# Performance work log

Hardware: AMD Instinct MI355X
Metric: run time of the kernel (lower is better)

Reference implementation:

```python
import jax, jax.numpy as jnp
import numpy as np

B, S, D, H = 4, 1024, 1024, 16
QL, KVL = 512, 256
NOPE, ROPE, VD = 64, 32, 64
E, TOPK, FE = 8, 2, 1024  # FE = intermediate_size // expert_num
EPS = 1e-6
NEG = -1e15

def rms_norm(x, w):
    var = jnp.mean(x * x, axis=-1, keepdims=True)
    return w * (x * jax.lax.rsqrt(var + EPS))

def rotate_half(x):
    x1, x2 = jnp.split(x, 2, axis=-1)
    return jnp.concatenate([-x2, x1], axis=-1)

def rope_tables(seq_len, dim):
    inv = 1.0 / (10000.0 ** (np.arange(0, dim, 2, dtype=np.float32) / dim))
    freqs = np.arange(seq_len, dtype=np.float32)[:, None] @ inv[None, :]
    freqs = np.concatenate([freqs, freqs], axis=-1)
    return jnp.asarray(np.cos(freqs)), jnp.asarray(np.sin(freqs))

def setup_inputs():
    key = jax.random.key(0)
    ks = jax.random.split(key, 12)
    s = 0.02
    return {
        'hidden_state': jax.random.normal(ks[0], (B, S, D), jnp.float32),
        'attention_mask': jnp.ones((B, S), jnp.int32),
        'in_ln_w': jnp.ones((D,), jnp.float32),
        'post_ln_w': jnp.ones((D,), jnp.float32),
        'wq_a_w': jax.random.normal(ks[1], (QL, D)) * s,
        'wq_a_b': jnp.zeros((QL,), jnp.float32),
        'q_norm_w': jnp.ones((QL,), jnp.float32),
        'wq_b_w': jax.random.normal(ks[2], (H * (NOPE + ROPE), QL)) * s,
        'wq_b_b': jnp.zeros((H * (NOPE + ROPE),), jnp.float32),
        'wkv_a_w': jax.random.normal(ks[3], (KVL + ROPE, D)) * s,
        'wkv_a_b': jnp.zeros((KVL + ROPE,), jnp.float32),
        'kv_norm_w': jnp.ones((KVL,), jnp.float32),
        'wkv_b_w': jax.random.normal(ks[4], (H * (NOPE + VD), KVL)) * s,
        'wo_w': jax.random.normal(ks[5], (D, H * VD)) * s,
        'wo_b': jnp.zeros((D,), jnp.float32),
        'gate_w': jax.random.normal(ks[6], (E, D)) * s,
        'gate_b': jnp.zeros((E,), jnp.float32),
        'gate_proj': jax.random.normal(ks[7], (E, FE, D)) * s,
        'up_proj': jax.random.normal(ks[8], (E, FE, D)) * s,
        'down_proj': jax.random.normal(ks[9], (E, D, FE)) * s,
    }

def _forward(hidden_state, in_ln_w, post_ln_w, wq_a_w, wq_a_b, q_norm_w, wq_b_w, wq_b_b,
             wkv_a_w, wkv_a_b, kv_norm_w, wkv_b_w, wo_w, wo_b,
             gate_w, gate_b, gate_proj, up_proj, down_proj, attention_mask):
    x = rms_norm(hidden_state, in_ln_w)
    # ---- MLA ----
    q = rms_norm(x @ wq_a_w.T + wq_a_b, q_norm_w)
    q = (q @ wq_b_w.T + wq_b_b).reshape(B, S, H, NOPE + ROPE)
    q_nope, q_pe = q[..., :NOPE], q[..., NOPE:]
    kvp = x @ wkv_a_w.T + wkv_a_b
    kv, k_pe = kvp[..., :KVL], kvp[..., KVL:]
    kv = rms_norm(kv, kv_norm_w)
    cos, sin = rope_tables(S, ROPE)
    cos = cos[None, :, None, :]
    sin = sin[None, :, None, :]
    q_pe = q_pe * cos + rotate_half(q_pe) * sin            # [B,S,H,ROPE]
    k_pe = k_pe[:, :, None, :]
    k_pe = (k_pe * cos + rotate_half(k_pe) * sin)[:, :, 0]  # [B,S,ROPE]
    # kv_cache / pe_cache are filled with detached copies in the original
    kv_c = jax.lax.stop_gradient(kv)
    pe_c = jax.lax.stop_gradient(k_pe)
    wkv_b = wkv_b_w.reshape(H, NOPE + VD, KVL)
    q_abs = jnp.einsum('bshd,hdc->bshc', q_nope, wkv_b[:, :NOPE])  # cache-absorption
    scores = (jnp.einsum('bshc,btc->bsht', q_abs, kv_c)
              + jnp.einsum('bshr,btr->bsht', q_pe, pe_c)) / np.float32(np.sqrt(NOPE + ROPE))
    causal = jnp.triu(jnp.full((S, S), NEG, dtype=scores.dtype), 1)
    mask = jnp.where((attention_mask == 0)[:, None, :], NEG, causal[None])  # [B,S,S]
    scores = scores + mask[:, :, None, :]
    probs = jax.nn.softmax(scores, axis=-1)
    o = jnp.einsum('bsht,btc->bshc', probs, kv_c)
    o = jnp.einsum('bshc,hdc->bshd', o, wkv_b[:, NOPE:])
    attn = o.reshape(B, S, H * VD) @ wo_w.T + wo_b
    h = attn + hidden_state
    # ---- MoE ----
    y = rms_norm(h, post_ln_w)
    logits = y @ gate_w.T + gate_b                                   # [B,S,E]
    _, idx = jax.lax.top_k(logits, TOPK)
    sel = jnp.any(jax.nn.one_hot(idx, E, dtype=bool), axis=-2)       # [B,S,E]
    sparse = jax.nn.softmax(jnp.where(sel, logits, -jnp.inf), axis=-1)  # zeros off top-k
    g = jax.nn.silu(jnp.einsum('bsd,efd->bsef', y, gate_proj))
    u = jnp.einsum('bsd,efd->bsef', y, up_proj)
    eo = jnp.einsum('bsef,edf->bsed', g * u, down_proj)
    moe_out = jnp.einsum('bsed,bse->bsd', eo, sparse)
    out = moe_out + h
    return out, logits.reshape(-1, E)

def reference(hidden_state, attention_mask, in_ln_w, post_ln_w, wq_a_w, wq_a_b, q_norm_w,
              wq_b_w, wq_b_b, wkv_a_w, wkv_a_b, kv_norm_w, wkv_b_w, wo_w, wo_b,
              gate_w, gate_b, gate_proj, up_proj, down_proj):
    return _forward(hidden_state, in_ln_w, post_ln_w, wq_a_w, wq_a_b, q_norm_w, wq_b_w, wq_b_b,
                    wkv_a_w, wkv_a_b, kv_norm_w, wkv_b_w, wo_w, wo_b,
                    gate_w, gate_b, gate_proj, up_proj, down_proj, attention_mask)
```

## Files before the change

kernel.cpp:

```cpp
#include <hip/hip_runtime.h>
#include <math.h>

#define NB   4
#define NS   1024
#define ND   1024
#define NH   16
#define NTOK 4096
#define NFE  1024
#define ETOK_CAP 10240

#define SCL_LOG2E 0.14724445f

static constexpr size_t OFF_GWP  = 0;
static constexpr size_t OFF_TKW  = 8192;
static constexpr size_t OFF_EW   = 16384;
static constexpr size_t OFF_INT  = 26624;
static constexpr size_t OFF_X    = 45184;
static constexpr size_t OFF_QA   = 2142336;
static constexpr size_t OFF_GATE = 2142336;
static constexpr size_t OFF_UP   = 6336640;
static constexpr size_t OFF_QAB  = 8433792;
static constexpr size_t OFF_KVP  = 9482368;
static constexpr size_t OFF_KVC  = 10662016;
static constexpr size_t OFF_WA   = 11251840;
// ... 106 lines not shown
#pragma unroll
    for (int j = 0; j < 4; j++) acc[i][j] = (f32x4_t){0.f, 0.f, 0.f, 0.f};

  ld(0); st();
  __syncthreads();
  for (int k0 = 0; ; ) {
    int kn = k0 + 64;
    if (kn < K) ld(kn);
#pragma unroll
    for (int kk = 0; kk < 2; kk++) {
      bf16x8_t af[4], wf[4];
#pragma unroll
      for (int i = 0; i < 4; i++)
        af[i] = *(const bf16x8_t*)&As[(mw + 16*i + lr) * GSTR + kk*32 + lg*8];
#pragma unroll
      for (int j = 0; j < 4; j++)
        wf[j] = *(const bf16x8_t*)&Ws2[(nw + 16*j + lr) * GSTR + kk*32 + lg*8];
#pragma unroll
      for (int i = 0; i < 4; i++)
#pragma unroll
        for (int j = 0; j < 4; j++)
          acc[i][j] = __builtin_amdgcn_mfma_f32_16x16x32_bf16(af[i], wf[j], acc[i][j], 0, 0, 0);
    }
    k0 = kn;
    if (k0 >= K) break;
    __syncthreads();
    st();
    __syncthreads();
  }
#pragma unroll
  for (int j = 0; j < 4; j++) {
    int n = n0 + nw + 16*j + lr;
    if (n < N) {
      float bv = bias[n];
#pragma unroll
      for (int i = 0; i < 4; i++) {
#pragma unroll
        for (int r = 0; r < 4; r++) {
          int m = m0 + mw + 16*i + 4*lg + r;
          size_t off = (size_t)m * ldc + n;
          float v = acc[i][j][r] + bv;
          if (RESID) v += resid[off];
          if (OUTBF) ((unsigned short*)Cv)[off] = f2bfs(v);
          else       ((float*)Cv)[off] = v;
        }
      }
    }
  }
}

__global__ __launch_bounds__(256) void rope_q_kernel(float* qbuf)
{
  int id = blockIdx.x * 256 + threadIdx.x;
  int d = id & 15;
  int h = (id >> 4) & 15;
  int sr = id >> 8;
  int s = sr & (NS - 1);
  float inv = __expf(-(float)(2 * d) * (9.210340371976184f / 32.f));
  float fr = (float)s * inv;
  float sn, cs; sincosf(fr, &sn, &cs);
  float* p = qbuf + (size_t)sr * 1536 + h * 96 + 64;
  float x1 = p[d], x2 = p[d + 16];
  p[d]      = x1 * cs - x2 * sn;
  p[d + 16] = x2 * cs + x1 * sn;
}

__global__ __launch_bounds__(256) void rope_k_kernel(const float* kvp, unsigned short* kvc)
{
  int id = blockIdx.x * 256 + threadIdx.x;
  int d = id & 15;
  int sr = id >> 4;
  int s = sr & (NS - 1);
  float inv = __expf(-(float)(2 * d) * (9.210340371976184f / 32.f));
  float fr = (float)s * inv;
  float sn, cs; sincosf(fr, &sn, &cs);
  const float* src = kvp + (size_t)sr * 288 + 256;
  unsigned short* dst = kvc + (size_t)sr * 288 + 256;
  float x1 = src[d], x2 = src[d + 16];
  dst[d]      = f2bfs(x1 * cs - x2 * sn);
  dst[d + 16] = f2bfs(x2 * cs + x1 * sn);
}

#define KSTR 296
#define QNSTR 65
#define VPAD 40
#define OSTR2 132

__global__ __launch_bounds__(256, 2) void attn_kernel(
    const float* __restrict__ qbuf,
    const unsigned short* __restrict__ kvc,
    const float* __restrict__ wkvb,
    unsigned short* __restrict__ oproj)
{
  extern __shared__ float4 smem_f4[];
  unsigned short* sm  = (unsigned short*)smem_f4;
  unsigned short* ks  = sm;
  unsigned short* vt  = sm + 9472;
  unsigned short* ps  = sm + 19712;
  float* qn           = (float*)sm;
  unsigned short* qst = sm + 8320;
  float* o_lds        = (float*)sm;

  int bx = blockIdx.x;
  int h = blockIdx.y, b = blockIdx.z;
  int t = threadIdx.x;
  int lane = t & 63, wv_ = t >> 6;
  int lrow = lane & 15, lg = lane >> 4;
  int qrow = 16 * wv_ + lrow;

  int srow[5], sc16[5];
#pragma unroll
  for (int it = 0; it < 5; it++) {
    int c = it * 256 + t;
    srow[it] = c / 36; sc16[it] = c % 36;
  }
  bool tail = (t < 128);

  for (int half = 0; half < 2; half++) {
    int qb = half ? bx : (15 - bx);
    int row0 = b * NS + qb * 64;
    __syncthreads();

    for (int idx = t; idx < 4096; idx += 256) {
      int r = idx >> 6, c = idx & 63;
      qn[r * QNSTR + c] = qbuf[(size_t)(row0 + r) * 1536 + h * 96 + c] * SCL_LOG2E;
    }
    bf16x8_t bq[9];
    {
      const float* src = qbuf + (size_t)(row0 + qrow) * 1536 + h * 96 + 64 + lg * 8;
      unsigned short* bp = (unsigned short*)&bq[8];
#pragma unroll
      for (int j = 0; j < 8; j++) bp[j] = f2bfs(src[j] * SCL_LOG2E);
    }
    __syncthreads();
    {
      int cx = t & 63, ry = t >> 6;
      float a[16][4] = {};
      const float* wb = wkvb + (size_t)h * 32768 + cx * 4;
      for (int k = 0; k < 64; k++) {
        float4 wv = *(const float4*)(wb + (size_t)k * 256);
#pragma unroll
        for (int r = 0; r < 16; r++) {
          float qv = qn[(ry * 16 + r) * QNSTR + k];
          a[r][0] += qv * wv.x; a[r][1] += qv * wv.y; a[r][2] += qv * wv.z; a[r][3] += qv * wv.w;
        }
      }
      __syncthreads();
#pragma unroll
      for (int r = 0; r < 16; r++) {
        uint2 pk; pk.x = pack2(a[r][0], a[r][1]); pk.y = pack2(a[r][2], a[r][3]);
        *(uint2*)&qst[(ry * 16 + r) * KSTR + cx * 4] = pk;
      }
    }
    __syncthreads();
#pragma unroll
    for (int kk = 0; kk < 8; kk++)
      bq[kk] = *(const bf16x8_t*)&qst[qrow * KSTR + kk * 32 + lg * 8];
    __syncthreads();

    float m_run = -1e30f, l_run = 0.f;
    f32x4_t acco[16];
#pragma unroll
    for (int n = 0; n < 16; n++) acco[n] = (f32x4_t){0.f, 0.f, 0.f, 0.f};

    uint4 pa[5];
    unsigned short vg[32];

    auto issue = [&](int kb2) {
      const unsigned short* tb = kvc + ((size_t)b * NS + kb2 * 32) * 288;
#pragma unroll
      for (int it = 0; it < 4; it++)
        pa[it] = *(const uint4*)(tb + srow[it] * 288 + sc16[it] * 8);
      if (tail) pa[4] = *(const uint4*)(tb + srow[4] * 288 + sc16[4] * 8);
      const unsigned short* vsrc = tb + t;
#pragma unroll
      for (int k = 0; k < 32; k++) vg[k] = vsrc[k * 288];
    };
    auto commit = [&]() {
#pragma unroll
      for (int it = 0; it < 5; it++) {
        if (it == 4 && !tail) continue;
        *(uint4*)&ks[srow[it] * KSTR + sc16[it] * 8] = pa[it];
      }
      unsigned wds[16];
#pragma unroll
      for (int j = 0; j < 16; j++)
        wds[j] = (unsigned)vg[2*j] | ((unsigned)vg[2*j+1] << 16);
#pragma unroll
      for (int j = 0; j < 4; j++)
        *(uint4*)&vt[t * VPAD + j * 8] =
          make_uint4(wds[4*j], wds[4*j+1], wds[4*j+2], wds[4*j+3]);
    };

    int nkb = 2 * qb + 2;
    issue(0); commit();
    __syncthreads();
    for (int kb = 0; kb < nkb; kb++) {
      bool more = (kb + 1 < nkb);
      if (more) issue(kb + 1);
      int key0 = kb * 32;
      f32x4_t s0e = {0.f,0.f,0.f,0.f}, s0o = {0.f,0.f,0.f,0.f};
      f32x4_t s1e = {0.f,0.f,0.f,0.f}, s1o = {0.f,0.f,0.f,0.f};
#pragma unroll
      for (int kk = 0; kk < 9; kk++) {
        bf16x8_t a0 = *(const bf16x8_t*)&ks[lrow * KSTR + kk*32 + lg*8];
        bf16x8_t a1 = *(const bf16x8_t*)&ks[(16 + lrow) * KSTR + kk*32 + lg*8];
        if (kk & 1) {
          s0o = __builtin_amdgcn_mfma_f32_16x16x32_bf16(a0, bq[kk], s0o, 0, 0, 0);
          s1o = __builtin_amdgcn_mfma_f32_16x16x32_bf16(a1, bq[kk], s1o, 0, 0, 0);
        } else {
          s0e = __builtin_amdgcn_mfma_f32_16x16x32_bf16(a0, bq[kk], s0e, 0, 0, 0);
          s1e = __builtin_amdgcn_mfma_f32_16x16x32_bf16(a1, bq[kk], s1e, 0, 0, 0);
        }
      }
      f32x4_t s0a = s0e + s0o, s1a = s1e + s1o;
      int qg = qb * 64 + qrow;
      float sv[8];
      if (key0 + 31 > qb * 64 + 16 * wv_) {
#pragma unroll
        for (int r = 0; r < 4; r++) {
          sv[r]     = (key0 + 4*lg + r      <= qg) ? s0a[r] : -1e30f;
          sv[4 + r] = (key0 + 16 + 4*lg + r <= qg) ? s1a[r] : -1e30f;
        }
      } else {
#pragma unroll
        for (int r = 0; r < 4; r++) { sv[r] = s0a[r]; sv[4 + r] = s1a[r]; }
      }
      float mx = sv[0];
#pragma unroll
      for (int i = 1; i < 8; i++) mx = fmaxf(mx, sv[i]);
      mx = fmaxf(mx, __shfl_xor(mx, 16));
      mx = fmaxf(mx, __shfl_xor(mx, 32));
      if (!__all(mx - m_run <= 11.0f)) {
        float mnew = fmaxf(m_run, mx);
        float al = exp2f(m_run - mnew);
        m_run = mnew;
        l_run *= al;
        float al0 = __shfl(al, 4*lg + 0);
        float al1 = __shfl(al, 4*lg + 1);
        float al2 = __shfl(al, 4*lg + 2);
        float al3 = __shfl(al, 4*lg + 3);
#pragma unroll
        for (int n = 0; n < 16; n++) {
          acco[n][0] *= al0; acco[n][1] *= al1; acco[n][2] *= al2; acco[n][3] *= al3;
        }
      }
      float sum = 0.f;
#pragma unroll
      for (int i = 0; i < 8; i++) { sv[i] = exp2f(sv[i] - m_run); sum += sv[i]; }
      sum += __shfl_xor(sum, 16);
      sum += __shfl_xor(sum, 32);
      l_run += sum;
      {
        int swz = qrow & 3;
        int g0 = lg >> 1, h0 = lg & 1;
        uint2 p0; p0.x = pack2(sv[0], sv[1]); p0.y = pack2(sv[2], sv[3]);
        uint2 p1; p1.x = pack2(sv[4], sv[5]); p1.y = pack2(sv[6], sv[7]);
        char* pr = (char*)ps + qrow * 64;
        *(uint2*)(pr + ((g0 ^ swz) * 16 + h0 * 8))       = p0;
        *(uint2*)(pr + (((2 + g0) ^ swz) * 16 + h0 * 8)) = p1;
      }
      {
        bf16x8_t ap = *(const bf16x8_t*)((char*)ps + qrow * 64 + ((lg ^ (qrow & 3)) * 16));
#pragma unroll
        for (int n = 0; n < 16; n++) {
          bf16x8_t bv = *(const bf16x8_t*)&vt[(16*n + lrow) * VPAD + lg * 8];
          acco[n] = __builtin_amdgcn_mfma_f32_16x16x32_bf16(ap, bv, acco[n], 0, 0, 0);
        }
      }
      __syncthreads();
      if (more) { commit(); __syncthreads(); }
    }
    float li = 1.f / l_run;
    float l0 = __shfl(li, 4*lg + 0);
    float l1 = __shfl(li, 4*lg + 1);
    float l2 = __shfl(li, 4*lg + 2);
    float l3 = __shfl(li, 4*lg + 3);
    int dx = t & 15, ty2 = t >> 4;
    float pr[4][4] = {};
    const float* wb2 = wkvb + (size_t)(h * 128 + 64) * 256;
#pragma unroll
    for (int p = 0; p < 2; p++) {
      __syncthreads();
#pragma unroll
      for (int n = 8*p; n < 8*p + 8; n++) {
        int fc = 16*n + lrow - 128*p;
        o_lds[(16*wv_ + 4*lg + 0) * OSTR2 + fc] = acco[n][0] * l0;
        o_lds[(16*wv_ + 4*lg + 1) * OSTR2 + fc] = acco[n][1] * l1;
        o_lds[(16*wv_ + 4*lg + 2) * OSTR2 + fc] = acco[n][2] * l2;
        o_lds[(16*wv_ + 4*lg + 3) * OSTR2 + fc] = acco[n][3] * l3;
      }
      __syncthreads();
      for (int c = 0; c < 128; c += 4) {
        float4 w0 = *(const float4*)(wb2 + (size_t)(dx*4 + 0) * 256 + 128*p + c);
        float4 w1 = *(const float4*)(wb2 + (size_t)(dx*4 + 1) * 256 + 128*p + c);
        float4 w2 = *(const float4*)(wb2 + (size_t)(dx*4 + 2) * 256 + 128*p + c);
        float4 w3 = *(const float4*)(wb2 + (size_t)(dx*4 + 3) * 256 + 128*p + c);
#pragma unroll
        for (int i = 0; i < 4; i++) {
          float4 ov = *(const float4*)&o_lds[(ty2*4 + i) * OSTR2 + c];
          pr[i][0] += ov.x*w0.x + ov.y*w0.y + ov.z*w0.z + ov.w*w0.w;
          pr[i][1] += ov.x*w1.x + ov.y*w1.y + ov.z*w1.z + ov.w*w1.w;
          pr[i][2] += ov.x*w2.x + ov.y*w2.y + ov.z*w2.z + ov.w*w2.w;
          pr[i][3] += ov.x*w3.x + ov.y*w3.y + ov.z*w3.z + ov.w*w3.w;
        }
      }
    }
#pragma unroll
    for (int i = 0; i < 4; i++)
#pragma unroll
      for (int j = 0; j < 4; j++)
        oproj[(size_t)(row0 + ty2*4 + i) * 1024 + h * 64 + dx*4 + j] = f2bfs(pr[i][j]);
  }
}

__global__ __launch_bounds__(256) void gate_kernel(
    const float* __restrict__ H, const float* __restrict__ gwp,
    const float* __restrict__ gb, float* __restrict__ logits)
{
  __shared__ __align__(16) float ly[1024];
  __shared__ float red[4];
  int tok = blockIdx.x, t = threadIdx.x;
  float4 hv = *(const float4*)(H + (size_t)tok * ND + t * 4);
  *(float4*)&ly[t * 4] = hv;
  float ss = hv.x*hv.x + hv.y*hv.y + hv.z*hv.z + hv.w*hv.w;
#pragma unroll
  for (int k = 1; k < 64; k <<= 1) ss += __shfl_xor(ss, k);
  if ((t & 63) == 0) red[t >> 6] = ss;
  __syncthreads();
  float inv = rsqrtf((red[0] + red[1] + red[2] + red[3]) * (1.f / 1024.f) + 1e-6f);
  int e = t >> 5, lane = t & 31;
  const float* w = gwp + (size_t)e * ND;
  float acc = 0.f;
  for (int d = lane; d < ND; d += 32) acc += ly[d] * w[d];
#pragma unroll
  for (int k = 16; k >= 1; k >>= 1) acc += __shfl_xor(acc, k);
  if (lane == 0) logits[(size_t)tok * 8 + e] = acc * inv + gb[e];
}

__global__ __launch_bounds__(256) void topk_kernel(
    const float* __restrict__ logits, int* __restrict__ tke,
    float* __restrict__ tkw, int* __restrict__ cnt)
{
  int tok = blockIdx.x * 256 + threadIdx.x;
  if (tok >= NTOK) return;
  float l[8];
#pragma unroll
  for (int e2 = 0; e2 < 8; e2++) l[e2] = logits[(size_t)tok * 8 + e2];
  float v0 = l[0]; int e0 = 0;
#pragma unroll
  for (int e2 = 1; e2 < 8; e2++) if (l[e2] > v0) { v0 = l[e2]; e0 = e2; }
  float v1 = -INFINITY; int e1 = 0;
#pragma unroll
  for (int e2 = 0; e2 < 8; e2++) if (e2 != e0 && l[e2] > v1) { v1 = l[e2]; e1 = e2; }
  float x = __expf(v1 - v0);
  float w0 = 1.f / (1.f + x);
  tke[tok * 2]     = e0; tke[tok * 2 + 1] = e1;
  tkw[tok * 2]     = w0; tkw[tok * 2 + 1] = 1.f - w0;
  atomicAdd(&cnt[e0], 1);
  atomicAdd(&cnt[8 + e1], 1);
}

__global__ void offsets_kernel(const int* cnt, int* base, int* pcnt)
{
  if (threadIdx.x == 0 && blockIdx.x == 0) {
    int cum = 0;
    for (int s2 = 0; s2 < 16; s2++) {
      int p = (cnt[s2] + 127) & ~127;
      base[s2] = cum; pcnt[s2] = p; cum += p;
    }
  }
}

__global__ __launch_bounds__(256) void scatter_kernel(
    const int* __restrict__ tke, const float* __restrict__ tkw,
    const int* __restrict__ base, int* cnt2,
    int* __restrict__ etok, float* __restrict__ ew)
{
  int tok = blockIdx.x * 256 + threadIdx.x;
  if (tok >= NTOK) return;
#pragma unroll
  for (int k = 0; k < 2; k++) {
    int e = tke[tok * 2 + k];
    int seg = k * 8 + e;
    int pos = atomicAdd(&cnt2[seg], 1);
    int row = base[seg] + pos;
    etok[row] = tok;
    ew[row] = tkw[tok * 2 + k];
  }
}

#define MSTR 40

__global__ __launch_bounds__(256) void moe_mlp1_mfma(
    const unsigned short* __restrict__ Y,
    const unsigned short* __restrict__ Gp, const unsigned short* __restrict__ Up,
    const int* __restrict__ etok, const int* __restrict__ base,
    const int* __restrict__ pcnt, unsigned short* __restrict__ act)
{
  int seg = blockIdx.z;
  if ((int)(blockIdx.y * 128) >= pcnt[seg]) return;
  int e = seg & 7;
  __shared__ __align__(16) unsigned short As[128 * MSTR];
  __shared__ __align__(16) unsigned short Gs[128 * MSTR];
  __shared__ __align__(16) unsigned short Us[128 * MSTR];
  int t = threadIdx.x;
  int row0 = base[seg] + blockIdx.y * 128;
  int n0 = blockIdx.x * 128;
  int lane = t & 63, w = t >> 6;
  int mw = (w >> 1) * 64, nw = (w & 1) * 64;
  int lr = lane & 15, lg = lane >> 4;

  int srowv[2], sc8v[2];
#pragma unroll
  for (int it = 0; it < 2; it++) { int c = it*256 + t; srowv[it] = c >> 2; sc8v[it] = (c & 3) * 8; }
  int tokr[2];
#pragma unroll
  for (int it = 0; it < 2; it++) tokr[it] = etok[row0 + srowv[it]];

  uint4 pa[2], pg[2], pu[2];
  auto ld = [&](int k0) {
#pragma unroll
    for (int it = 0; it < 2; it++) {
      pa[it] = (tokr[it] >= 0)
        ? *(const uint4*)(Y + (size_t)tokr[it] * ND + k0 + sc8v[it])
        : make_uint4(0u, 0u, 0u, 0u);
      pg[it] = *(const uint4*)(Gp + ((size_t)e * NFE + n0 + srowv[it]) * ND + k0 + sc8v[it]);
      pu[it] = *(const uint4*)(Up + ((size_t)e * NFE + n0 + srowv[it]) * ND + k0 + sc8v[it]);
    }
  };
  auto st = [&]() {
#pragma unroll
    for (int it = 0; it < 2; it++) {
      *(uint4*)&As[srowv[it] * MSTR + sc8v[it]] = pa[it];
      *(uint4*)&Gs[srowv[it] * MSTR + sc8v[it]] = pg[it];
      *(uint4*)&Us[srowv[it] * MSTR + sc8v[it]] = pu[it];
    }
  };

  f32x4_t accg[4][4], accu[4][4];
#pragma unroll
  for (int i = 0; i < 4; i++)
#pragma unroll
    for (int j = 0; j < 4; j++) {
      accg[i][j] = (f32x4_t){0.f, 0.f, 0.f, 0.f};
      accu[i][j] = (f32x4_t){0.f, 0.f, 0.f, 0.f};
    }

  ld(0); st();
  __syncthreads();
  for (int k0 = 0; ; ) {
    int kn = k0 + 32;
    if (kn < ND) ld(kn);
    bf16x8_t af[4], gf[4], uf[4];
#pragma unroll
    for (int i = 0; i < 4; i++)
      af[i] = *(const bf16x8_t*)&As[(mw + 16*i + lr) * MSTR + lg*8];
#pragma unroll
    for (int j = 0; j < 4; j++) {
      gf[j] = *(const bf16x8_t*)&Gs[(nw + 16*j + lr) * MSTR + lg*8];
      uf[j] = *(const bf16x8_t*)&Us[(nw + 16*j + lr) * MSTR + lg*8];
    }
#pragma unroll
    for (int i = 0; i < 4; i++)
#pragma unroll
      for (int j = 0; j < 4; j++) {
        accg[i][j] = __builtin_amdgcn_mfma_f32_16x16x32_bf16(af[i], gf[j], accg[i][j], 0, 0, 0);
        accu[i][j] = __builtin_amdgcn_mfma_f32_16x16x32_bf16(af[i], uf[j], accu[i][j], 0, 0, 0);
      }
    k0 = kn;
    if (k0 >= ND) break;
    __syncthreads();
    st();
    __syncthreads();
  }
#pragma unroll
  for (int i = 0; i < 4; i++)
#pragma unroll
    for (int j = 0; j < 4; j++) {
      int n = n0 + nw + 16*j + lr;
#pragma unroll
      for (int r = 0; r < 4; r++) {
        int m = row0 + mw + 16*i + 4*lg + r;
        float g = accg[i][j][r], u = accu[i][j][r];
        float s = g / (1.f + __expf(-g));
        act[(size_t)m * NFE + n] = f2bfs(s * u);
      }
    }
}

__global__ __launch_bounds__(256) void moe_down_mfma(
    const unsigned short* __restrict__ act, const unsigned short* __restrict__ Dp,
    const int* __restrict__ etok, const float* __restrict__ ew,
    const int* __restrict__ base, const int* __restrict__ pcnt,
    int slot, float* __restrict__ out)
{
  int e = blockIdx.z;
  int seg = slot * 8 + e;
  if ((int)(blockIdx.y * 128) >= pcnt[seg]) return;
  __shared__ __align__(16) unsigned short As[128 * GSTR];
  __shared__ __align__(16) unsigned short Ws2[128 * GSTR];
  int t = threadIdx.x;
  int row0 = base[seg] + blockIdx.y * 128;
  int n0 = blockIdx.x * 128;
  int lane = t & 63, w = t >> 6;
  int mw = (w >> 1) * 64, nw = (w & 1) * 64;
  int lr = lane & 15, lg = lane >> 4;

  int srowv[4], sc8v[4];
#pragma unroll
  for (int it = 0; it < 4; it++) { int c = it*256 + t; srowv[it] = c >> 3; sc8v[it] = (c & 7) * 8; }

  uint4 pa[4], pw[4];
  auto ld = [&](int k0) {
#pragma unroll
    for (int it = 0; it < 4; it++) {
      pa[it] = *(const uint4*)(act + (size_t)(row0 + srowv[it]) * NFE + k0 + sc8v[it]);
      pw[it] = *(const uint4*)(Dp + ((size_t)e * ND + n0 + srowv[it]) * NFE + k0 + sc8v[it]);
    }
  };
  auto st = [&]() {
#pragma unroll
    for (int it = 0; it < 4; it++) {
      *(uint4*)&As[srowv[it] * GSTR + sc8v[it]] = pa[it];
      *(uint4*)&Ws2[srowv[it] * GSTR + sc8v[it]] = pw[it];
    }
  };

  f32x4_t acc[4][4];
#pragma unroll
  for (int i = 0; i < 4; i++)
#pragma unroll
    for (int j = 0; j < 4; j++) acc[i][j] = (f32x4_t){0.f, 0.f, 0.f, 0.f};

  ld(0); st();
  __syncthreads();
  for (int k0 = 0; ; ) {
    int kn = k0 + 64;
    if (kn < NFE) ld(kn);
#pragma unroll
    for (int kk = 0; kk < 2; kk++) {
      bf16x8_t af[4], wf[4];
#pragma unroll
      for (int i = 0; i < 4; i++)
        af[i] = *(const bf16x8_t*)&As[(mw + 16*i + lr) * GSTR + kk*32 + lg*8];
#pragma unroll
      for (int j = 0; j < 4; j++)
        wf[j] = *(const bf16x8_t*)&Ws2[(nw + 16*j + lr) * GSTR + kk*32 + lg*8];
#pragma unroll
      for (int i = 0; i < 4; i++)
#pragma unroll
        for (int j = 0; j < 4; j++)
          acc[i][j] = __builtin_amdgcn_mfma_f32_16x16x32_bf16(af[i], wf[j], acc[i][j], 0, 0, 0);
    }
    k0 = kn;
    if (k0 >= NFE) break;
    __syncthreads();
    st();
    __syncthreads();
  }
#pragma unroll
  for (int i = 0; i < 4; i++) {
// ... 10 lines not shown
      for (int r = 0; r < 4; r++) {
        if (tks[r] >= 0)
          out[(size_t)tks[r] * ND + n] += ews[r] * acc[i][j][r];
      }
    }
  }
}

extern "C" void kernel_launch(void* const* d_in, const int* in_sizes, int n_in,
                              void* d_out, int out_size, void* d_ws, size_t ws_size,
                              hipStream_t stream) {
  const float* hidden    = (const float*)d_in[0];
  const float* in_ln_w   = (const float*)d_in[2];
  const float* post_ln_w = (const float*)d_in[3];
  const float* wq_a_w    = (const float*)d_in[4];
  const float* wq_a_b    = (const float*)d_in[5];
  const float* q_norm_w  = (const float*)d_in[6];
  const float* wq_b_w    = (const float*)d_in[7];
  const float* wq_b_b    = (const float*)d_in[8];
  const float* wkv_a_w   = (const float*)d_in[9];
  const float* wkv_a_b   = (const float*)d_in[10];
  const float* kv_norm_w = (const float*)d_in[11];
  const float* wkv_b_w   = (const float*)d_in[12];
  const float* wo_w      = (const float*)d_in[13];
  const float* wo_b      = (const float*)d_in[14];
  const float* gate_w    = (const float*)d_in[15];
  const float* gate_b    = (const float*)d_in[16];
  const float* gate_proj = (const float*)d_in[17];
  const float* up_proj   = (const float*)d_in[18];
  const float* down_proj = (const float*)d_in[19];

  float* ws = (float*)d_ws;
  if (ws_size < WS_FLOATS * sizeof(float)) return;

  float* gwp = ws + OFF_GWP;
  float* tkw = ws + OFF_TKW;
  float* ew  = ws + OFF_EW;
  int* ib   = (int*)(ws + OFF_INT);
  int* tke  = ib;
  int* etok = ib + 8192;
  int* cnt  = ib + 8192 + ETOK_CAP;
  int* cnt2 = cnt + 16;
  int* base = cnt + 32;
  int* pcnt = cnt + 48;

  unsigned short* x_bf   = (unsigned short*)(ws + OFF_X);
  unsigned short* oproj  = (unsigned short*)(ws + OFF_X);
  unsigned short* ybuf   = (unsigned short*)(ws + OFF_X);
  float*          qa     = ws + OFF_QA;
  float*          qbuf   = ws + OFF_QA;
  unsigned short* gate_bf= (unsigned short*)(ws + OFF_GATE);
  unsigned short* down_bf= (unsigned short*)(ws + OFF_GATE);
  unsigned short* up_bf  = (unsigned short*)(ws + OFF_UP);
  unsigned short* qab    = (unsigned short*)(ws + OFF_QAB);
  float*          kvp    = ws + OFF_KVP;
  unsigned short* kvc    = (unsigned short*)(ws + OFF_KVC);
  unsigned short* actb   = (unsigned short*)(ws + OFF_ACT);
  unsigned short* wqa_bf = (unsigned short*)(ws + OFF_WA + WA_WQA);
  unsigned short* wqb_bf = (unsigned short*)(ws + OFF_WA + WA_WQB);
  unsigned short* wkva_bf= (unsigned short*)(ws + OFF_WA + WA_WKVA);
  unsigned short* wo_bf  = (unsigned short*)(ws + OFF_WA + WA_WO);

  float* out    = (float*)d_out;
  float* logits = out + (size_t)NTOK * ND;

  conv_bf16_kernel<<<256, 256, 0, stream>>>(wq_a_w, wqa_bf, 524288);
  conv_bf16_kernel<<<144, 256, 0, stream>>>(wkv_a_w, wkva_bf, 294912);
  conv_bf16_kernel<<<384, 256, 0, stream>>>(wq_b_w, wqb_bf, 786432);
  conv_bf16_kernel<<<512, 256, 0, stream>>>(wo_w, wo_bf, 1048576);
  conv_gwp_kernel<<<32, 256, 0, stream>>>(gate_w, post_ln_w, gwp);

  rmsnorm_bf16<4><<<NTOK, 256, 0, stream>>>(hidden, ND, in_ln_w, x_bf, ND);
  gemm_bf16<false,false><<<dim3(4, 32), 256, 0, stream>>>(
      x_bf, ND, wqa_bf, ND, wq_a_b, nullptr, qa, 512, 512, ND);
  gemm_bf16<false,false><<<dim3(3, 32), 256, 0, stream>>>(
      x_bf, ND, wkva_bf, ND, wkv_a_b, nullptr, kvp, 288, 288, ND);
  rmsnorm_bf16<2><<<NTOK, 256, 0, stream>>>(qa, 512, q_norm_w, qab, 512);
  rmsnorm_bf16<1><<<NTOK, 256, 0, stream>>>(kvp, 288, kv_norm_w, kvc, 288);
  gemm_bf16<false,false><<<dim3(12, 32), 256, 0, stream>>>(
      qab, 512, wqb_bf, 512, wq_b_b, nullptr, qbuf, 1536, 1536, 512);
  rope_q_kernel<<<4096, 256, 0, stream>>>(qbuf);
  rope_k_kernel<<<256, 256, 0, stream>>>(kvp, kvc);
  {
    size_t smem = 54528;
    hipFuncSetAttribute((const void*)attn_kernel,
                        hipFuncAttributeMaxDynamicSharedMemorySize, (int)smem);
    attn_kernel<<<dim3(8, NH, NB), 256, smem, stream>>>(qbuf, kvc, wkv_b_w, oproj);
  }
  conv_bf16_kernel<<<4096, 256, 0, stream>>>(gate_proj, gate_bf, 8388608);
  conv_bf16_kernel<<<4096, 256, 0, stream>>>(up_proj, up_bf, 8388608);
  gemm_bf16<false,true><<<dim3(8, 32), 256, 0, stream>>>(
      oproj, ND, wo_bf, ND, wo_b, hidden, out, ND, ND, ND);
  rmsnorm_bf16<4><<<NTOK, 256, 0, stream>>>(out, ND, post_ln_w, ybuf, ND);
  gate_kernel<<<NTOK, 256, 0, stream>>>(out, gwp, gate_b, logits);
  hipMemsetAsync(cnt, 0, 32 * sizeof(int), stream);
  hipMemsetAsync(etok, 0xFF, ETOK_CAP * sizeof(int), stream);
  topk_kernel<<<16, 256, 0, stream>>>(logits, tke, tkw, cnt);
  offsets_kernel<<<1, 64, 0, stream>>>(cnt, base, pcnt);
  scatter_kernel<<<16, 256, 0, stream>>>(tke, tkw, base, cnt2, etok, ew);
  moe_mlp1_mfma<<<dim3(8, 32, 16), 256, 0, stream>>>(ybuf, gate_bf, up_bf,
                                                     etok, base, pcnt, actb);
  conv_bf16_kernel<<<4096, 256, 0, stream>>>(down_proj, down_bf, 8388608);
  moe_down_mfma<<<dim3(8, 32, 8), 256, 0, stream>>>(actb, down_bf, etok, ew,
                                                    base, pcnt, 0, out);
  moe_down_mfma<<<dim3(8, 32, 8), 256, 0, stream>>>(actb, down_bf, etok, ew,
                                                    base, pcnt, 1, out);
}
```

Baseline: 1.012 ms.

## Split attention blocks to one query tile each and retile MoE gate/up GEMM

The attention kernel no longer pairs two causal query tiles per block. It launches one block per 64-row query tile and raises the occupancy hint to 3 blocks per CU, relying on the reversed tile order for load balance. The q-norm staging stride drops its padding, which may add LDS bank conflicts. The MoE gate/up kernel moves from 128x128 to 128x64 N-tiles with a 64-wide K step, so twice as many blocks launch with fewer accumulators each, but the activation tile is reloaded across more N-blocks.

```diff
diff --git a/kernel.cpp b/kernel.cpp
--- a/kernel.cpp
+++ b/kernel.cpp
@@ -212,11 +212,11 @@
 }
 
 #define KSTR 296
-#define QNSTR 65
+#define QNSTR 64
 #define VPAD 40
 #define OSTR2 132
 
-__global__ __launch_bounds__(256, 2) void attn_kernel(
+__global__ __launch_bounds__(256, 3) void attn_kernel(
     const float* __restrict__ qbuf,
     const unsigned short* __restrict__ kvc,
     const float* __restrict__ wkvb,
@@ -228,16 +228,58 @@
   unsigned short* vt  = sm + 9472;
   unsigned short* ps  = sm + 19712;
   float* qn           = (float*)sm;
-  unsigned short* qst = sm + 8320;
+  unsigned short* qst = sm + 8192;
   float* o_lds        = (float*)sm;
 
-  int bx = blockIdx.x;
+  int qb = (NS / 64 - 1) - blockIdx.x;
   int h = blockIdx.y, b = blockIdx.z;
   int t = threadIdx.x;
+  int row0 = b * NS + qb * 64;
   int lane = t & 63, wv_ = t >> 6;
   int lrow = lane & 15, lg = lane >> 4;
   int qrow = 16 * wv_ + lrow;
 
+  for (int idx = t; idx < 4096; idx += 256) {
+    int r = idx >> 6, c = idx & 63;
+    qn[r * QNSTR + c] = qbuf[(size_t)(row0 + r) * 1536 + h * 96 + c] * SCL_LOG2E;
+  }
+  bf16x8_t bq[9];
+  {
+    const float* src = qbuf + (size_t)(row0 + qrow) * 1536 + h * 96 + 64 + lg * 8;
+    unsigned short* bp = (unsigned short*)&bq[8];
+#pragma unroll
+    for (int j = 0; j < 8; j++) bp[j] = f2bfs(src[j] * SCL_LOG2E);
+  }
+  __syncthreads();
+  {
+    int cx = t & 63, ry = t >> 6;
+    float a[16][4] = {};
+    const float* wb = wkvb + (size_t)h * 32768 + cx * 4;
+    for (int k = 0; k < 64; k++) {
+      float4 wv = *(const float4*)(wb + (size_t)k * 256);
+#pragma unroll
+      for (int r = 0; r < 16; r++) {
+        float qv = qn[(ry * 16 + r) * QNSTR + k];
+        a[r][0] += qv * wv.x; a[r][1] += qv * wv.y; a[r][2] += qv * wv.z; a[r][3] += qv * wv.w;
+      }
+    }
+#pragma unroll
+    for (int r = 0; r < 16; r++) {
+      uint2 pk; pk.x = pack2(a[r][0], a[r][1]); pk.y = pack2(a[r][2], a[r][3]);
+      *(uint2*)&qst[(ry * 16 + r) * KSTR + cx * 4] = pk;
+    }
+  }
+  __syncthreads();
+#pragma unroll
+  for (int kk = 0; kk < 8; kk++)
+    bq[kk] = *(const bf16x8_t*)&qst[qrow * KSTR + kk * 32 + lg * 8];
+  __syncthreads();
+
+  float m_run = -1e30f, l_run = 0.f;
+  f32x4_t acco[16];
+#pragma unroll
+  for (int n = 0; n < 16; n++) acco[n] = (f32x4_t){0.f, 0.f, 0.f, 0.f};
+
   int srow[5], sc16[5];
 #pragma unroll
   for (int it = 0; it < 5; it++) {
@@ -245,203 +287,154 @@
     srow[it] = c / 36; sc16[it] = c % 36;
   }
   bool tail = (t < 128);
-
-  for (int half = 0; half < 2; half++) {
-    int qb = half ? bx : (15 - bx);
-    int row0 = b * NS + qb * 64;
+  uint4 pa[5];
+  unsigned short vg[32];
+
+  auto issue = [&](int kb2) {
+    const unsigned short* tb = kvc + ((size_t)b * NS + kb2 * 32) * 288;
+#pragma unroll
+    for (int it = 0; it < 4; it++)
+      pa[it] = *(const uint4*)(tb + srow[it] * 288 + sc16[it] * 8);
+    if (tail) pa[4] = *(const uint4*)(tb + srow[4] * 288 + sc16[4] * 8);
+    const unsigned short* vsrc = tb + t;
+#pragma unroll
+    for (int k = 0; k < 32; k++) vg[k] = vsrc[k * 288];
+  };
+  auto commit = [&]() {
+#pragma unroll
+    for (int it = 0; it < 5; it++) {
+      if (it == 4 && !tail) continue;
+      *(uint4*)&ks[srow[it] * KSTR + sc16[it] * 8] = pa[it];
+    }
+    unsigned wds[16];
+#pragma unroll
+    for (int j = 0; j < 16; j++)
+      wds[j] = (unsigned)vg[2*j] | ((unsigned)vg[2*j+1] << 16);
+#pragma unroll
+    for (int j = 0; j < 4; j++)
+      *(uint4*)&vt[t * VPAD + j * 8] =
+        make_uint4(wds[4*j], wds[4*j+1], wds[4*j+2], wds[4*j+3]);
+  };
+
+  int nkb = 2 * qb + 2;
+  issue(0); commit();
+  __syncthreads();
+  for (int kb = 0; kb < nkb; kb++) {
+    bool more = (kb + 1 < nkb);
+    if (more) issue(kb + 1);
+    int key0 = kb * 32;
+    f32x4_t s0e = {0.f,0.f,0.f,0.f}, s0o = {0.f,0.f,0.f,0.f};
+    f32x4_t s1e = {0.f,0.f,0.f,0.f}, s1o = {0.f,0.f,0.f,0.f};
+#pragma unroll
+    for (int kk = 0; kk < 9; kk++) {
+      bf16x8_t a0 = *(const bf16x8_t*)&ks[lrow * KSTR + kk*32 + lg*8];
+      bf16x8_t a1 = *(const bf16x8_t*)&ks[(16 + lrow) * KSTR + kk*32 + lg*8];
+      if (kk & 1) {
+        s0o = __builtin_amdgcn_mfma_f32_16x16x32_bf16(a0, bq[kk], s0o, 0, 0, 0);
+        s1o = __builtin_amdgcn_mfma_f32_16x16x32_bf16(a1, bq[kk], s1o, 0, 0, 0);
+      } else {
+        s0e = __builtin_amdgcn_mfma_f32_16x16x32_bf16(a0, bq[kk], s0e, 0, 0, 0);
+        s1e = __builtin_amdgcn_mfma_f32_16x16x32_bf16(a1, bq[kk], s1e, 0, 0, 0);
+      }
+    }
+    f32x4_t s0a = s0e + s0o, s1a = s1e + s1o;
+    int qg = qb * 64 + qrow;
+    float sv[8];
+    if (key0 + 31 > qb * 64 + 16 * wv_) {
+#pragma unroll
+      for (int r = 0; r < 4; r++) {
+        sv[r]     = (key0 + 4*lg + r      <= qg) ? s0a[r] : -1e30f;
+        sv[4 + r] = (key0 + 16 + 4*lg + r <= qg) ? s1a[r] : -1e30f;
+      }
+    } else {
+#pragma unroll
+      for (int r = 0; r < 4; r++) { sv[r] = s0a[r]; sv[4 + r] = s1a[r]; }
+    }
+    float mx = sv[0];
+#pragma unroll
+    for (int i = 1; i < 8; i++) mx = fmaxf(mx, sv[i]);
+    mx = fmaxf(mx, __shfl_xor(mx, 16));
+    mx = fmaxf(mx, __shfl_xor(mx, 32));
+    if (!__all(mx - m_run <= 11.0f)) {
+      float mnew = fmaxf(m_run, mx);
+      float al = exp2f(m_run - mnew);
+      m_run = mnew;
+      l_run *= al;
+      float al0 = __shfl(al, 4*lg + 0);
+      float al1 = __shfl(al, 4*lg + 1);
+      float al2 = __shfl(al, 4*lg + 2);
+      float al3 = __shfl(al, 4*lg + 3);
+#pragma unroll
+      for (int n = 0; n < 16; n++) {
+        acco[n][0] *= al0; acco[n][1] *= al1; acco[n][2] *= al2; acco[n][3] *= al3;
+      }
+    }
+    float sum = 0.f;
+#pragma unroll
+    for (int i = 0; i < 8; i++) { sv[i] = exp2f(sv[i] - m_run); sum += sv[i]; }
+    sum += __shfl_xor(sum, 16);
+    sum += __shfl_xor(sum, 32);
+    l_run += sum;
+    {
+      int swz = qrow & 3;
+      int g0 = lg >> 1, h0 = lg & 1;
+      uint2 p0; p0.x = pack2(sv[0], sv[1]); p0.y = pack2(sv[2], sv[3]);
+      uint2 p1; p1.x = pack2(sv[4], sv[5]); p1.y = pack2(sv[6], sv[7]);
+      char* pr = (char*)ps + qrow * 64;
+      *(uint2*)(pr + ((g0 ^ swz) * 16 + h0 * 8))       = p0;
+      *(uint2*)(pr + (((2 + g0) ^ swz) * 16 + h0 * 8)) = p1;
+    }
+    {
+      bf16x8_t ap = *(const bf16x8_t*)((char*)ps + qrow * 64 + ((lg ^ (qrow & 3)) * 16));
+#pragma unroll
+      for (int n = 0; n < 16; n++) {
+        bf16x8_t bv = *(const bf16x8_t*)&vt[(16*n + lrow) * VPAD + lg * 8];
+        acco[n] = __builtin_amdgcn_mfma_f32_16x16x32_bf16(ap, bv, acco[n], 0, 0, 0);
+      }
+    }
     __syncthreads();
-
-    for (int idx = t; idx < 4096; idx += 256) {
-      int r = idx >> 6, c = idx & 63;
-      qn[r * QNSTR + c] = qbuf[(size_t)(row0 + r) * 1536 + h * 96 + c] * SCL_LOG2E;
-    }
-    bf16x8_t bq[9];
-    {
-      const float* src = qbuf + (size_t)(row0 + qrow) * 1536 + h * 96 + 64 + lg * 8;
-      unsigned short* bp = (unsigned short*)&bq[8];
-#pragma unroll
-      for (int j = 0; j < 8; j++) bp[j] = f2bfs(src[j] * SCL_LOG2E);
-    }
+    if (more) { commit(); __syncthreads(); }
+  }
+  float li = 1.f / l_run;
+  float l0 = __shfl(li, 4*lg + 0);
+  float l1 = __shfl(li, 4*lg + 1);
+  float l2 = __shfl(li, 4*lg + 2);
+  float l3 = __shfl(li, 4*lg + 3);
+  int dx = t & 15, ty2 = t >> 4;
+  float pr[4][4] = {};
+  const float* wb2 = wkvb + (size_t)(h * 128 + 64) * 256;
+#pragma unroll
+  for (int p = 0; p < 2; p++) {
     __syncthreads();
-    {
-      int cx = t & 63, ry = t >> 6;
-      float a[16][4] = {};
-      const float* wb = wkvb + (size_t)h * 32768 + cx * 4;
-      for (int k = 0; k < 64; k++) {
-        float4 wv = *(const float4*)(wb + (size_t)k * 256);
-#pragma unroll
-        for (int r = 0; r < 16; r++) {
-          float qv = qn[(ry * 16 + r) * QNSTR + k];
-          a[r][0] += qv * wv.x; a[r][1] += qv * wv.y; a[r][2] += qv * wv.z; a[r][3] += qv * wv.w;
-        }
-      }
-      __syncthreads();
-#pragma unroll
-      for (int r = 0; r < 16; r++) {
-        uint2 pk; pk.x = pack2(a[r][0], a[r][1]); pk.y = pack2(a[r][2], a[r][3]);
-        *(uint2*)&qst[(ry * 16 + r) * KSTR + cx * 4] = pk;
-      }
+#pragma unroll
+    for (int n = 8*p; n < 8*p + 8; n++) {
+      int fc = 16*n + lrow - 128*p;
+      o_lds[(16*wv_ + 4*lg + 0) * OSTR2 + fc] = acco[n][0] * l0;
+      o_lds[(16*wv_ + 4*lg + 1) * OSTR2 + fc] = acco[n][1] * l1;
+      o_lds[(16*wv_ + 4*lg + 2) * OSTR2 + fc] = acco[n][2] * l2;
+      o_lds[(16*wv_ + 4*lg + 3) * OSTR2 + fc] = acco[n][3] * l3;
     }
     __syncthreads();
-#pragma unroll
-    for (int kk = 0; kk < 8; kk++)
-      bq[kk] = *(const bf16x8_t*)&qst[qrow * KSTR + kk * 32 + lg * 8];
-    __syncthreads();
-
-    float m_run = -1e30f, l_run = 0.f;
-    f32x4_t acco[16];
-#pragma unroll
-    for (int n = 0; n < 16; n++) acco[n] = (f32x4_t){0.f, 0.f, 0.f, 0.f};
-
-    uint4 pa[5];
-    unsigned short vg[32];
-
-    auto issue = [&](int kb2) {
-      const unsigned short* tb = kvc + ((size_t)b * NS + kb2 * 32) * 288;
-#pragma unroll
-      for (int it = 0; it < 4; it++)
-        pa[it] = *(const uint4*)(tb + srow[it] * 288 + sc16[it] * 8);
-      if (tail) pa[4] = *(const uint4*)(tb + srow[4] * 288 + sc16[4] * 8);
-      const unsigned short* vsrc = tb + t;
-#pragma unroll
-      for (int k = 0; k < 32; k++) vg[k] = vsrc[k * 288];
-    };
-    auto commit = [&]() {
-#pragma unroll
-      for (int it = 0; it < 5; it++) {
-        if (it == 4 && !tail) continue;
-        *(uint4*)&ks[srow[it] * KSTR + sc16[it] * 8] = pa[it];
-      }
-      unsigned wds[16];
-#pragma unroll
-      for (int j = 0; j < 16; j++)
-        wds[j] = (unsigned)vg[2*j] | ((unsigned)vg[2*j+1] << 16);
-#pragma unroll
-      for (int j = 0; j < 4; j++)
-        *(uint4*)&vt[t * VPAD + j * 8] =
-          make_uint4(wds[4*j], wds[4*j+1], wds[4*j+2], wds[4*j+3]);
-    };
-
-    int nkb = 2 * qb + 2;
-    issue(0); commit();
-    __syncthreads();
-    for (int kb = 0; kb < nkb; kb++) {
-      bool more = (kb + 1 < nkb);
-      if (more) issue(kb + 1);
-      int key0 = kb * 32;
-      f32x4_t s0e = {0.f,0.f,0.f,0.f}, s0o = {0.f,0.f,0.f,0.f};
-      f32x4_t s1e = {0.f,0.f,0.f,0.f}, s1o = {0.f,0.f,0.f,0.f};
-#pragma unroll
-      for (int kk = 0; kk < 9; kk++) {
-        bf16x8_t a0 = *(const bf16x8_t*)&ks[lrow * KSTR + kk*32 + lg*8];
-        bf16x8_t a1 = *(const bf16x8_t*)&ks[(16 + lrow) * KSTR + kk*32 + lg*8];
-        if (kk & 1) {
-          s0o = __builtin_amdgcn_mfma_f32_16x16x32_bf16(a0, bq[kk], s0o, 0, 0, 0);
-          s1o = __builtin_amdgcn_mfma_f32_16x16x32_bf16(a1, bq[kk], s1o, 0, 0, 0);
-        } else {
-          s0e = __builtin_amdgcn_mfma_f32_16x16x32_bf16(a0, bq[kk], s0e, 0, 0, 0);
-          s1e = __builtin_amdgcn_mfma_f32_16x16x32_bf16(a1, bq[kk], s1e, 0, 0, 0);
-        }
-      }
-      f32x4_t s0a = s0e + s0o, s1a = s1e + s1o;
-      int qg = qb * 64 + qrow;
-      float sv[8];
-      if (key0 + 31 > qb * 64 + 16 * wv_) {
-#pragma unroll
-        for (int r = 0; r < 4; r++) {
-          sv[r]     = (key0 + 4*lg + r      <= qg) ? s0a[r] : -1e30f;
-          sv[4 + r] = (key0 + 16 + 4*lg + r <= qg) ? s1a[r] : -1e30f;
-        }
-      } else {
-#pragma unroll
-        for (int r = 0; r < 4; r++) { sv[r] = s0a[r]; sv[4 + r] = s1a[r]; }
-      }
-      float mx = sv[0];
-#pragma unroll
-      for (int i = 1; i < 8; i++) mx = fmaxf(mx, sv[i]);
-      mx = fmaxf(mx, __shfl_xor(mx, 16));
-      mx = fmaxf(mx, __shfl_xor(mx, 32));
-      if (!__all(mx - m_run <= 11.0f)) {
-        float mnew = fmaxf(m_run, mx);
-        float al = exp2f(m_run - mnew);
-        m_run = mnew;
-        l_run *= al;
-        float al0 = __shfl(al, 4*lg + 0);
-        float al1 = __shfl(al, 4*lg + 1);
-        float al2 = __shfl(al, 4*lg + 2);
-        float al3 = __shfl(al, 4*lg + 3);
-#pragma unroll
-        for (int n = 0; n < 16; n++) {
-          acco[n][0] *= al0; acco[n][1] *= al1; acco[n][2] *= al2; acco[n][3] *= al3;
-        }
-      }
-      float sum = 0.f;
-#pragma unroll
-      for (int i = 0; i < 8; i++) { sv[i] = exp2f(sv[i] - m_run); sum += sv[i]; }
-      sum += __shfl_xor(sum, 16);
-      sum += __shfl_xor(sum, 32);
-      l_run += sum;
-      {
-        int swz = qrow & 3;
-        int g0 = lg >> 1, h0 = lg & 1;
-        uint2 p0; p0.x = pack2(sv[0], sv[1]); p0.y = pack2(sv[2], sv[3]);
-        uint2 p1; p1.x = pack2(sv[4], sv[5]); p1.y = pack2(sv[6], sv[7]);
-        char* pr = (char*)ps + qrow * 64;
-        *(uint2*)(pr + ((g0 ^ swz) * 16 + h0 * 8))       = p0;
-        *(uint2*)(pr + (((2 + g0) ^ swz) * 16 + h0 * 8)) = p1;
-      }
-      {
-        bf16x8_t ap = *(const bf16x8_t*)((char*)ps + qrow * 64 + ((lg ^ (qrow & 3)) * 16));
-#pragma unroll
-        for (int n = 0; n < 16; n++) {
-          bf16x8_t bv = *(const bf16x8_t*)&vt[(16*n + lrow) * VPAD + lg * 8];
-          acco[n] = __builtin_amdgcn_mfma_f32_16x16x32_bf16(ap, bv, acco[n], 0, 0, 0);
-        }
-      }
-      __syncthreads();
-      if (more) { commit(); __syncthreads(); }
-    }
-    float li = 1.f / l_run;
-    float l0 = __shfl(li, 4*lg + 0);
-    float l1 = __shfl(li, 4*lg + 1);
-    float l2 = __shfl(li, 4*lg + 2);
-    float l3 = __shfl(li, 4*lg + 3);
-    int dx = t & 15, ty2 = t >> 4;
-    float pr[4][4] = {};
-    const float* wb2 = wkvb + (size_t)(h * 128 + 64) * 256;
-#pragma unroll
-    for (int p = 0; p < 2; p++) {
-      __syncthreads();
-#pragma unroll
-      for (int n = 8*p; n < 8*p + 8; n++) {
-        int fc = 16*n + lrow - 128*p;
-        o_lds[(16*wv_ + 4*lg + 0) * OSTR2 + fc] = acco[n][0] * l0;
-        o_lds[(16*wv_ + 4*lg + 1) * OSTR2 + fc] = acco[n][1] * l1;
-        o_lds[(16*wv_ + 4*lg + 2) * OSTR2 + fc] = acco[n][2] * l2;
-        o_lds[(16*wv_ + 4*lg + 3) * OSTR2 + fc] = acco[n][3] * l3;
-      }
-      __syncthreads();
-      for (int c = 0; c < 128; c += 4) {
-        float4 w0 = *(const float4*)(wb2 + (size_t)(dx*4 + 0) * 256 + 128*p + c);
-        float4 w1 = *(const float4*)(wb2 + (size_t)(dx*4 + 1) * 256 + 128*p + c);
-        float4 w2 = *(const float4*)(wb2 + (size_t)(dx*4 + 2) * 256 + 128*p + c);
-        float4 w3 = *(const float4*)(wb2 + (size_t)(dx*4 + 3) * 256 + 128*p + c);
-#pragma unroll
-        for (int i = 0; i < 4; i++) {
-          float4 ov = *(const float4*)&o_lds[(ty2*4 + i) * OSTR2 + c];
-          pr[i][0] += ov.x*w0.x + ov.y*w0.y + ov.z*w0.z + ov.w*w0.w;
-          pr[i][1] += ov.x*w1.x + ov.y*w1.y + ov.z*w1.z + ov.w*w1.w;
-          pr[i][2] += ov.x*w2.x + ov.y*w2.y + ov.z*w2.z + ov.w*w2.w;
-          pr[i][3] += ov.x*w3.x + ov.y*w3.y + ov.z*w3.z + ov.w*w3.w;
-        }
-      }
-    }
-#pragma unroll
-    for (int i = 0; i < 4; i++)
-#pragma unroll
-      for (int j = 0; j < 4; j++)
-        oproj[(size_t)(row0 + ty2*4 + i) * 1024 + h * 64 + dx*4 + j] = f2bfs(pr[i][j]);
-  }
+    for (int c = 0; c < 128; c += 4) {
+      float4 w0 = *(const float4*)(wb2 + (size_t)(dx*4 + 0) * 256 + 128*p + c);
+      float4 w1 = *(const float4*)(wb2 + (size_t)(dx*4 + 1) * 256 + 128*p + c);
+      float4 w2 = *(const float4*)(wb2 + (size_t)(dx*4 + 2) * 256 + 128*p + c);
+      float4 w3 = *(const float4*)(wb2 + (size_t)(dx*4 + 3) * 256 + 128*p + c);
+#pragma unroll
+      for (int i = 0; i < 4; i++) {
+        float4 ov = *(const float4*)&o_lds[(ty2*4 + i) * OSTR2 + c];
+        pr[i][0] += ov.x*w0.x + ov.y*w0.y + ov.z*w0.z + ov.w*w0.w;
+        pr[i][1] += ov.x*w1.x + ov.y*w1.y + ov.z*w1.z + ov.w*w1.w;
+        pr[i][2] += ov.x*w2.x + ov.y*w2.y + ov.z*w2.z + ov.w*w2.w;
+        pr[i][3] += ov.x*w3.x + ov.y*w3.y + ov.z*w3.z + ov.w*w3.w;
+      }
+    }
+  }
+#pragma unroll
+  for (int i = 0; i < 4; i++)
+#pragma unroll
+    for (int j = 0; j < 4; j++)
+      oproj[(size_t)(row0 + ty2*4 + i) * 1024 + h * 64 + dx*4 + j] = f2bfs(pr[i][j]);
 }
 
 __global__ __launch_bounds__(256) void gate_kernel(
@@ -520,9 +513,7 @@
   }
 }
 
-#define MSTR 40
-
-__global__ __launch_bounds__(256) void moe_mlp1_mfma(
+__global__ __launch_bounds__(256, 3) void moe_mlp1_mfma(
     const unsigned short* __restrict__ Y,
     const unsigned short* __restrict__ Gp, const unsigned short* __restrict__ Up,
     const int* __restrict__ etok, const int* __restrict__ base,
@@ -531,48 +522,51 @@
   int seg = blockIdx.z;
   if ((int)(blockIdx.y * 128) >= pcnt[seg]) return;
   int e = seg & 7;
-  __shared__ __align__(16) unsigned short As[128 * MSTR];
-  __shared__ __align__(16) unsigned short Gs[128 * MSTR];
-  __shared__ __align__(16) unsigned short Us[128 * MSTR];
+  __shared__ __align__(16) unsigned short As[128 * GSTR];
+  __shared__ __align__(16) unsigned short Gs[64 * GSTR];
+  __shared__ __align__(16) unsigned short Us[64 * GSTR];
   int t = threadIdx.x;
   int row0 = base[seg] + blockIdx.y * 128;
-  int n0 = blockIdx.x * 128;
+  int n0 = blockIdx.x * 64;
   int lane = t & 63, w = t >> 6;
-  int mw = (w >> 1) * 64, nw = (w & 1) * 64;
+  int mw = (w >> 1) * 64, nw = (w & 1) * 32;
   int lr = lane & 15, lg = lane >> 4;
 
-  int srowv[2], sc8v[2];
-#pragma unroll
-  for (int it = 0; it < 2; it++) { int c = it*256 + t; srowv[it] = c >> 2; sc8v[it] = (c & 3) * 8; }
-  int tokr[2];
-#pragma unroll
-  for (int it = 0; it < 2; it++) tokr[it] = etok[row0 + srowv[it]];
-
-  uint4 pa[2], pg[2], pu[2];
+  int srow = t >> 3, sc8 = (t & 7) * 8;
+  int tokr[4];
+#pragma unroll
+  for (int it = 0; it < 4; it++) tokr[it] = etok[row0 + it*32 + srow];
+
+  uint4 pa[4], pg[2], pu[2];
   auto ld = [&](int k0) {
 #pragma unroll
+    for (int it = 0; it < 4; it++)
+      pa[it] = (tokr[it] >= 0)
+        ? *(const uint4*)(Y + (size_t)tokr[it] * ND + k0 + sc8)
+        : make_uint4(0u, 0u, 0u, 0u);
+#pragma unroll
     for (int it = 0; it < 2; it++) {
-      pa[it] = (tokr[it] >= 0)
-        ? *(const uint4*)(Y + (size_t)tokr[it] * ND + k0 + sc8v[it])
-        : make_uint4(0u, 0u, 0u, 0u);
-      pg[it] = *(const uint4*)(Gp + ((size_t)e * NFE + n0 + srowv[it]) * ND + k0 + sc8v[it]);
-      pu[it] = *(const uint4*)(Up + ((size_t)e * NFE + n0 + srowv[it]) * ND + k0 + sc8v[it]);
+      int r = n0 + it*32 + srow;
+      pg[it] = *(const uint4*)(Gp + ((size_t)e * NFE + r) * ND + k0 + sc8);
+      pu[it] = *(const uint4*)(Up + ((size_t)e * NFE + r) * ND + k0 + sc8);
     }
   };
   auto st = [&]() {
 #pragma unroll
+    for (int it = 0; it < 4; it++)
+      *(uint4*)&As[(it*32 + srow) * GSTR + sc8] = pa[it];
+#pragma unroll
     for (int it = 0; it < 2; it++) {
-      *(uint4*)&As[srowv[it] * MSTR + sc8v[it]] = pa[it];
-      *(uint4*)&Gs[srowv[it] * MSTR + sc8v[it]] = pg[it];
-      *(uint4*)&Us[srowv[it] * MSTR + sc8v[it]] = pu[it];
+      *(uint4*)&Gs[(it*32 + srow) * GSTR + sc8] = pg[it];
+      *(uint4*)&Us[(it*32 + srow) * GSTR + sc8] = pu[it];
     }
   };
 
-  f32x4_t accg[4][4], accu[4][4];
+  f32x4_t accg[4][2], accu[4][2];
 #pragma unroll
   for (int i = 0; i < 4; i++)
 #pragma unroll
-    for (int j = 0; j < 4; j++) {
+    for (int j = 0; j < 2; j++) {
       accg[i][j] = (f32x4_t){0.f, 0.f, 0.f, 0.f};
       accu[i][j] = (f32x4_t){0.f, 0.f, 0.f, 0.f};
     }
@@ -580,24 +574,27 @@
   ld(0); st();
   __syncthreads();
   for (int k0 = 0; ; ) {
-    int kn = k0 + 32;
+    int kn = k0 + 64;
     if (kn < ND) ld(kn);
-    bf16x8_t af[4], gf[4], uf[4];
-#pragma unroll
-    for (int i = 0; i < 4; i++)
-      af[i] = *(const bf16x8_t*)&As[(mw + 16*i + lr) * MSTR + lg*8];
-#pragma unroll
-    for (int j = 0; j < 4; j++) {
-      gf[j] = *(const bf16x8_t*)&Gs[(nw + 16*j + lr) * MSTR + lg*8];
-      uf[j] = *(const bf16x8_t*)&Us[(nw + 16*j + lr) * MSTR + lg*8];
-    }
-#pragma unroll
-    for (int i = 0; i < 4; i++)
-#pragma unroll
-      for (int j = 0; j < 4; j++) {
-        accg[i][j] = __builtin_amdgcn_mfma_f32_16x16x32_bf16(af[i], gf[j], accg[i][j], 0, 0, 0);
-        accu[i][j] = __builtin_amdgcn_mfma_f32_16x16x32_bf16(af[i], uf[j], accu[i][j], 0, 0, 0);
-      }
+#pragma unroll
+    for (int kk = 0; kk < 2; kk++) {
+      bf16x8_t af[4], gf[2], uf[2];
+#pragma unroll
+      for (int i = 0; i < 4; i++)
+        af[i] = *(const bf16x8_t*)&As[(mw + 16*i + lr) * GSTR + kk*32 + lg*8];
+#pragma unroll
+      for (int j = 0; j < 2; j++) {
+        gf[j] = *(const bf16x8_t*)&Gs[(nw + 16*j + lr) * GSTR + kk*32 + lg*8];
+        uf[j] = *(const bf16x8_t*)&Us[(nw + 16*j + lr) * GSTR + kk*32 + lg*8];
+      }
+#pragma unroll
+      for (int i = 0; i < 4; i++)
+#pragma unroll
+        for (int j = 0; j < 2; j++) {
+          accg[i][j] = __builtin_amdgcn_mfma_f32_16x16x32_bf16(af[i], gf[j], accg[i][j], 0, 0, 0);
+          accu[i][j] = __builtin_amdgcn_mfma_f32_16x16x32_bf16(af[i], uf[j], accu[i][j], 0, 0, 0);
+        }
+    }
     k0 = kn;
     if (k0 >= ND) break;
     __syncthreads();
@@ -607,7 +604,7 @@
 #pragma unroll
   for (int i = 0; i < 4; i++)
 #pragma unroll
-    for (int j = 0; j < 4; j++) {
+    for (int j = 0; j < 2; j++) {
       int n = n0 + nw + 16*j + lr;
 #pragma unroll
       for (int r = 0; r < 4; r++) {
@@ -784,10 +781,10 @@
   rope_q_kernel<<<4096, 256, 0, stream>>>(qbuf);
   rope_k_kernel<<<256, 256, 0, stream>>>(kvp, kvc);
   {
-    size_t smem = 54528;
+    size_t smem = 54272;
     hipFuncSetAttribute((const void*)attn_kernel,
                         hipFuncAttributeMaxDynamicSharedMemorySize, (int)smem);
-    attn_kernel<<<dim3(8, NH, NB), 256, smem, stream>>>(qbuf, kvc, wkv_b_w, oproj);
+    attn_kernel<<<dim3(16, NH, NB), 256, smem, stream>>>(qbuf, kvc, wkv_b_w, oproj);
   }
   conv_bf16_kernel<<<4096, 256, 0, stream>>>(gate_proj, gate_bf, 8388608);
   conv_bf16_kernel<<<4096, 256, 0, stream>>>(up_proj, up_bf, 8388608);
@@ -800,8 +797,8 @@
   topk_kernel<<<16, 256, 0, stream>>>(logits, tke, tkw, cnt);
   offsets_kernel<<<1, 64, 0, stream>>>(cnt, base, pcnt);
   scatter_kernel<<<16, 256, 0, stream>>>(tke, tkw, base, cnt2, etok, ew);
-  moe_mlp1_mfma<<<dim3(8, 32, 16), 256, 0, stream>>>(ybuf, gate_bf, up_bf,
-                                                     etok, base, pcnt, actb);
+  moe_mlp1_mfma<<<dim3(16, 32, 16), 256, 0, stream>>>(ybuf, gate_bf, up_bf,
+                                                      etok, base, pcnt, actb);
   conv_bf16_kernel<<<4096, 256, 0, stream>>>(down_proj, down_bf, 8388608);
   moe_down_mfma<<<dim3(8, 32, 8), 256, 0, stream>>>(actb, down_bf, etok, ew,
                                                     base, pcnt, 0, out);
```

Result: slower. 1.203 ms (+18.8%).
